# Kernel optimization log

Hardware: AMD Instinct MI355X
Metric: run time of the kernel (lower is better)

## Reference

```python
import jax, jax.numpy as jnp
import numpy as np

GAMMA = 0.99
N_CODES = 1024  # module hardcodes self.N = 2**10

def setup_inputs() -> dict:
    key = jax.random.key(0)
    k1, k2, k3, k4 = jax.random.split(key, 4)
    B, D, S = 16, 256, 2048
    N_q = 8
    return {
        "data_object": jax.random.normal(k1, (B, D, S), dtype=jnp.float32),
        "codebooks": jax.random.normal(k2, (N_q, N_CODES, D), dtype=jnp.float32),
        "N_i": jax.random.uniform(k3, (N_q, N_CODES), dtype=jnp.float32),
        "m_i": jax.random.normal(k4, (N_q, N_CODES, D), dtype=jnp.float32),
    }

def reference(data_object, codebooks, N_i, m_i):
    # data_object: [b, D, s] -> y: [b, s, D]
    b, D, s = data_object.shape
    y = jnp.transpose(data_object, (0, 2, 1))

    def stage(carry, xs):
        residual, cur_y = carry          # [b, s, D] each
        W, Ni, mi = xs                   # [N, D], [N], [N, D]
        flat = residual.reshape(-1, D)   # [b*s, D]
        d2 = (jnp.sum(flat * flat, axis=-1, keepdims=True)
              + jnp.sum(W * W, axis=-1)[None, :]
              - 2.0 * flat @ W.T)
        idx = jnp.argmin(d2, axis=-1)    # [b*s]
        Q = W[idx].reshape(residual.shape)
        # EMA codebook statistics (bincount + index_add as segment sums)
        counts = jax.ops.segment_sum(jnp.ones(idx.shape, flat.dtype), idx, num_segments=N_CODES)
        vec = jax.ops.segment_sum(flat, idx, num_segments=N_CODES)
        new_N = Ni * GAMMA + counts * (1.0 - GAMMA)
        new_m = mi * GAMMA + vec * (1.0 - GAMMA)
        new_W = new_m / jnp.clip(new_N, 1e-8)[:, None]
        return (residual - Q, cur_y + Q), (idx.reshape(b, s), new_N, new_m, new_W)

    init = (y, jnp.zeros_like(y))
    (residual, cur_y), (indices, new_N, new_m, new_W) = jax.lax.scan(
        stage, init, (codebooks, N_i, m_i))

    # straight-through estimator + commitment loss
    logits = y + jax.lax.stop_gradient(cur_y - y)       # [b, s, D]
    commitment_loss = jnp.mean((jax.lax.stop_gradient(cur_y) - y) ** 2)
    logits = jnp.transpose(logits, (0, 2, 1))           # back to [b, D, s]
    return logits, commitment_loss, indices, new_N, new_m, new_W
```

## Files before the change

kernel.cpp:

```cpp
#include <hip/hip_runtime.h>
#include <hip/hip_bf16.h>


using f16   = _Float16;
using f16x4 = __attribute__((ext_vector_type(4))) _Float16;
using f16x8 = __attribute__((ext_vector_type(8))) _Float16;
using f32x4 = __attribute__((ext_vector_type(4))) float;
typedef unsigned long long u64;

#define GAMMA_F 0.99f
#define OMG_F   0.01f
#define LO_SCALE 1024.0f
#define LO_INV   (1.0f/1024.0f)

__global__ void sentinel_kernel(float* out, float v){
  if (threadIdx.x == 0 && blockIdx.x == 0) out[0] = v;
}

__global__ __launch_bounds__(64) void rownorm_kernel(const float* __restrict__ X,
                                                     float* __restrict__ out, int rows){
  int r = blockIdx.x;
  if (r >= rows) return;
  int l = threadIdx.x;
  const float* x = X + (size_t)r * 256;
  float s = 0.f;
  #pragma unroll
  for (int i = 0; i < 4; i++){ float v = x[l + i*64]; s += v*v; }
  #pragma unroll
  for (int o = 32; o > 0; o >>= 1) s += __shfl_down(s, o, 64);
  if (l == 0) out[r] = s;
}

__global__ __launch_bounds__(64) void wsplit_kernel(const float* __restrict__ W,
                                                    f16* __restrict__ frag){
  int blk = blockIdx.x;
  int lane = threadIdx.x;
  int code = (blk >> 3 << 4) + (lane & 15);
  int k0   = (blk & 7)*32 + (lane >> 4)*8;
  const float* src = W + (size_t)code * 256 + k0;
  float4 a = *(const float4*)(src);
  float4 b = *(const float4*)(src + 4);
  float x[8] = {a.x,a.y,a.z,a.w, b.x,b.y,b.z,b.w};
  f16x8 h8, l8;
  #pragma unroll
  for (int i = 0; i < 8; i++){
    f16 h = (f16)x[i];
    h8[i] = h;
    l8[i] = (f16)((x[i] - (float)h) * LO_SCALE);
  }
  f16* dst = frag + (size_t)blk * 1024 + lane*8;
  *(f16x8*)dst         = h8;
  *(f16x8*)(dst + 512) = l8;
}

__global__ __launch_bounds__(256) void init_kernel(const float* __restrict__ data,
                                                   f16* __restrict__ AH, f16* __restrict__ AL,
                                                   float* __restrict__ rnorm){
  __shared__ float rs[32][257];
  __shared__ float nrmp[32][8];
  int blk = blockIdx.x, b = blk >> 6, s0 = (blk & 63) * 32;
  int tid = threadIdx.x, c = tid & 31, g = tid >> 5;
  const float* dptr = data + (size_t)b * 524288 + s0;
  float np_ = 0.f;
  #pragma unroll 8
  for (int dd = 0; dd < 32; ++dd){
    int d = g*32 + dd;
    float x = dptr[(size_t)d * 2048 + c];
    rs[c][d] = x;
    np_ += x*x;
  }
  nrmp[c][g] = np_;
  __syncthreads();
  if (tid < 32){
    float s = 0.f;
    #pragma unroll
    for (int gg = 0; gg < 8; ++gg) s += nrmp[tid][gg];
    rnorm[blk*32 + tid] = s;
  }
  int r0 = blk*32;
  int c2 = tid >> 3, k0 = (tid & 7) * 32;
  #pragma unroll
  for (int jc = 0; jc < 4; ++jc){
    f16x8 h8, l8;
    #pragma unroll
    for (int j = 0; j < 8; ++j){
      float x = rs[c2][k0 + jc*8 + j];
      f16 h = (f16)x;
      h8[j] = h;
      l8[j] = (f16)((x - (float)h) * LO_SCALE);
    }
    size_t off = (size_t)(r0 + c2) * 256 + k0 + jc*8;
    *(f16x8*)(AH + off) = h8;
    *(f16x8*)(AL + off) = l8;
  }
}

__global__ __launch_bounds__(256) void out4init_kernel(const float* __restrict__ mi,
                                                       float* __restrict__ out4){
  int e4 = blockIdx.x*256 + threadIdx.x;
  float4 v = ((const float4*)mi)[e4];
  v.x *= GAMMA_F; v.y *= GAMMA_F; v.z *= GAMMA_F; v.w *= GAMMA_F;
  ((float4*)out4)[e4] = v;
}

__global__ __launch_bounds__(256, 2) void dist_kernel(
    const f16* __restrict__ AH, const f16* __restrict__ AL,
    const f16* __restrict__ whl, const float* __restrict__ wnorm,
    const float* __restrict__ rnorm, u64* __restrict__ keybuf, int q)
{
  __shared__ f16 Bs[2][16384];
  const int tid = threadIdx.x;
  const int lane = tid & 63;
  const int w = tid >> 6;
  const int rb = blockIdx.x, cs = blockIdx.y;
  const int rlo = lane & 15, kg = lane >> 4;
  const int T0 = rb*8 + w*2;

  f16x8 aH[2][8], aL[2][8];
  #pragma unroll
  for (int rt = 0; rt < 2; ++rt)
    #pragma unroll
    for (int kf = 0; kf < 8; ++kf){
      size_t off = (size_t)((T0+rt)*16 + rlo) * 256 + kf*32 + kg*8;
      aH[rt][kf] = *(const f16x8*)(AH + off);
      aL[rt][kf] = *(const f16x8*)(AL + off);
    }
  float rn[2][4];
  #pragma unroll
  for (int rt = 0; rt < 2; ++rt)
    #pragma unroll
    for (int i = 0; i < 4; ++i)
      rn[rt][i] = rnorm[(T0+rt)*16 + kg*4 + i];

  const f16* wb = whl + (size_t)q * 524288;
  const float* wn = wnorm + (q << 10);
  const int ct0 = cs * 16;

  float bestv[8]; int besti[8];
  #pragma unroll
  for (int r8_ = 0; r8_ < 8; ++r8_){ bestv[r8_] = 3.4e38f; besti[r8_] = 0; }

  {
    const f16* src = wb + (size_t)ct0 * 8192;
    f16x8 st[8];
    #pragma unroll
    for (int j = 0; j < 8; ++j) st[j] = *(const f16x8*)(src + tid*8 + j*2048);
    #pragma unroll
    for (int j = 0; j < 8; ++j) *(f16x8*)(&Bs[0][0] + tid*8 + j*2048) = st[j];
  }

  for (int it = 0; it < 8; ++it){
    int cb = ct0 + it*2;
    __syncthreads();
    f16x8 nx[8];
    if (it < 7){
      const f16* src = wb + (size_t)(cb+2) * 8192;
      #pragma unroll
      for (int j = 0; j < 8; ++j) nx[j] = *(const f16x8*)(src + tid*8 + j*2048);
    }
    #pragma unroll
    for (int sub = 0; sub < 2; ++sub){
      const f16* bb = &Bs[it & 1][0] + sub*8192;
      f32x4 hh[2], cr[2];
      #pragma unroll
      for (int rt = 0; rt < 2; ++rt){ hh[rt] = (f32x4)0.0f; cr[rt] = (f32x4)0.0f; }
      __builtin_amdgcn_s_setprio(1);
      #pragma unroll
      for (int kf = 0; kf < 8; ++kf){
        f16x8 bh = *(const f16x8*)(bb + kf*1024 + lane*8);
        f16x8 bl = *(const f16x8*)(bb + kf*1024 + 512 + lane*8);
        hh[0] = __builtin_amdgcn_mfma_f32_16x16x32_f16(aH[0][kf], bh, hh[0], 0,0,0);
        cr[0] = __builtin_amdgcn_mfma_f32_16x16x32_f16(aH[0][kf], bl, cr[0], 0,0,0);
        cr[0] = __builtin_amdgcn_mfma_f32_16x16x32_f16(aL[0][kf], bh, cr[0], 0,0,0);
        hh[1] = __builtin_amdgcn_mfma_f32_16x16x32_f16(aH[1][kf], bh, hh[1], 0,0,0);
        cr[1] = __builtin_amdgcn_mfma_f32_16x16x32_f16(aH[1][kf], bl, cr[1], 0,0,0);
        cr[1] = __builtin_amdgcn_mfma_f32_16x16x32_f16(aL[1][kf], bh, cr[1], 0,0,0);
      }
      __builtin_amdgcn_s_setprio(0);
      int code = ((cb + sub) << 4) + rlo;
      float wnc = wn[code];
      #pragma unroll
      for (int rt = 0; rt < 2; ++rt)
        #pragma unroll
        for (int i = 0; i < 4; ++i){
          float dot = hh[rt][i] + cr[rt][i] * LO_INV;
          float d2 = (rn[rt][i] + wnc) - 2.0f * dot;
          int r8_ = rt*4 + i;
          if (d2 < bestv[r8_] || (d2 == bestv[r8_] && code < besti[r8_])){
            bestv[r8_] = d2; besti[r8_] = code;
          }
        }
    }
    if (it < 7){
      #pragma unroll
      for (int j = 0; j < 8; ++j) *(f16x8*)(&Bs[(it+1) & 1][0] + tid*8 + j*2048) = nx[j];
    }
  }

  #pragma unroll
  for (int off = 1; off <= 8; off <<= 1){
    #pragma unroll
    for (int r8_ = 0; r8_ < 8; ++r8_){
      float ov = __shfl_xor(bestv[r8_], off, 16);
      int   oi = __shfl_xor(besti[r8_], off, 16);
      if (ov < bestv[r8_] || (ov == bestv[r8_] && oi < besti[r8_])){
        bestv[r8_] = ov; besti[r8_] = oi;
      }
    }
  }
  if (rlo == 0){
    #pragma unroll
    for (int r8_ = 0; r8_ < 8; ++r8_){
      int rt = r8_ >> 2, i = r8_ & 3;
      int grow = (T0 + rt)*16 + kg*4 + i;
      unsigned fb = __float_as_uint(bestv[r8_]);
      fb = (fb & 0x80000000u) ? ~fb : (fb | 0x80000000u);
      u64 key = ((u64)fb << 32) | (unsigned)besti[r8_];
      atomicMin(keybuf + grow, key);
    }
  }
}

__global__ __launch_bounds__(256) void hist_kernel(u64* __restrict__ keybuf,
                                                   float* __restrict__ out2q,
                                                   unsigned short* __restrict__ blockhist){
  __shared__ int h[1024];
  int tid = threadIdx.x, b = blockIdx.x;
  #pragma unroll
  for (int i = 0; i < 4; ++i) h[tid + 256*i] = 0;
  __syncthreads();
  #pragma unroll
  for (int j = 0; j < 4; ++j){
    int row = b*1024 + tid + 256*j;
    u64 k = keybuf[row];
    keybuf[row] = ~0ull;
    int c = (int)(k & 0xFFFF);
    out2q[row] = (float)c;
    atomicAdd(&h[c], 1);
  }
  __syncthreads();
  #pragma unroll
  for (int i = 0; i < 4; ++i)
    blockhist[b*1024 + tid + 256*i] = (unsigned short)h[tid + 256*i];
}

__global__ __launch_bounds__(256) void scanscatter_kernel(
    const unsigned short* __restrict__ blockhist, const float* __restrict__ out2q,
    unsigned short* __restrict__ rowlist, const float* __restrict__ Ni,
    float* __restrict__ out3, int q)
{
  __shared__ int wtot[4];
  __shared__ int cur[1024];
  int tid = threadIdx.x, b = blockIdx.x, lane = tid & 63, w = tid >> 6;
  const ushort4* bh4 = (const ushort4*)blockhist;
  int tot[4] = {0,0,0,0}, pre[4] = {0,0,0,0};
  for (int bb = 0; bb < 32; ++bb){
    ushort4 h = bh4[bb*256 + tid];
    if (bb < b){ pre[0]+=h.x; pre[1]+=h.y; pre[2]+=h.z; pre[3]+=h.w; }
    tot[0]+=h.x; tot[1]+=h.y; tot[2]+=h.z; tot[3]+=h.w;
  }
  int s = tot[0]+tot[1]+tot[2]+tot[3];
  int v = s;
  #pragma unroll
  for (int d = 1; d < 64; d <<= 1){
    int o = __shfl_up(v, d, 64);
    if (lane >= d) v += o;
  }
  if (lane == 63) wtot[w] = v;
  __syncthreads();
  int woff = 0;
  #pragma unroll
  for (int ww = 0; ww < 4; ++ww) if (ww < w) woff += wtot[ww];
  int base = woff + v - s;
  if (b == 0){
    const int qb = q << 10;
    out3[qb + 4*tid+0] = Ni[qb + 4*tid+0]*GAMMA_F + (float)tot[0]*OMG_F;
    out3[qb + 4*tid+1] = Ni[qb + 4*tid+1]*GAMMA_F + (float)tot[1]*OMG_F;
    out3[qb + 4*tid+2] = Ni[qb + 4*tid+2]*GAMMA_F + (float)tot[2]*OMG_F;
    out3[qb + 4*tid+3] = Ni[qb + 4*tid+3]*GAMMA_F + (float)tot[3]*OMG_F;
  }
  cur[4*tid+0] = base + pre[0];
  cur[4*tid+1] = base + tot[0] + pre[1];
  cur[4*tid+2] = base + tot[0]+tot[1] + pre[2];
  cur[4*tid+3] = base + tot[0]+tot[1]+tot[2] + pre[3];
  __syncthreads();
  #pragma unroll
  for (int j = 0; j < 4; ++j){
    int row = b*1024 + tid + 256*j;
    int c = (int)out2q[row];
    int pos = atomicAdd(&cur[c], 1);
    rowlist[pos] = (unsigned short)row;
  }
}

__global__ __launch_bounds__(64) void update_kernel(
    f16* __restrict__ AH, f16* __restrict__ AL,
    const unsigned short* __restrict__ rowlist, const float* __restrict__ out2q,
    const float* __restrict__ codebooks, float* __restrict__ out4,
    float* __restrict__ rnorm, int q)
{
  const int lane = threadIdx.x;
  const int s0 = blockIdx.x * 16;
  int myrow = 0, mycode = 0;
  if (lane < 16){
    myrow = rowlist[s0 + lane];
    mycode = (int)out2q[myrow];
  }
  float vs[4] = {0.f, 0.f, 0.f, 0.f};
  float Wk[4] = {0.f, 0.f, 0.f, 0.f};
  int prev = -1;
  int rowp = __shfl(myrow, 0, 64);
  f16x4 ph = *(const f16x4*)(AH + (size_t)rowp*256 + lane*4);
  f16x4 pl = *(const f16x4*)(AL + (size_t)rowp*256 + lane*4);
  for (int s = 0; s < 16; ++s){
    int row  = __shfl(myrow, s, 64);
    int code = __shfl(mycode, s, 64);
    f16x4 h4 = ph, l4 = pl;
    if (s < 15){
      int rown = __shfl(myrow, s+1, 64);
      ph = *(const f16x4*)(AH + (size_t)rown*256 + lane*4);
      pl = *(const f16x4*)(AL + (size_t)rown*256 + lane*4);
    }
    if (code != prev){
      if (prev >= 0){
        float* dst = out4 + (((size_t)q << 10) + prev)*256 + lane*4;
        #pragma unroll
        for (int t = 0; t < 4; ++t) atomicAdd(dst + t, vs[t] * OMG_F);
      }
      float4 wv = *(const float4*)&codebooks[(((size_t)q << 10) + code)*256 + lane*4];
      Wk[0] = wv.x; Wk[1] = wv.y; Wk[2] = wv.z; Wk[3] = wv.w;
      vs[0] = vs[1] = vs[2] = vs[3] = 0.f;
      prev = code;
    }
    size_t base = (size_t)row * 256 + lane*4;
    f16x4 nh, nl;
    float p = 0.f;
    #pragma unroll
    for (int t = 0; t < 4; ++t){
      float rj = (float)h4[t] + (float)l4[t] * LO_INV;
      vs[t] += rj;
      float rn_ = rj - Wk[t];
      f16 hh = (f16)rn_;
      nh[t] = hh;
      nl[t] = (f16)((rn_ - (float)hh) * LO_SCALE);
      p += rn_ * rn_;
    }
    *(f16x4*)(AH + base) = nh;
    *(f16x4*)(AL + base) = nl;
    #pragma unroll
    for (int o = 32; o > 0; o >>= 1) p += __shfl_down(p, o, 64);
    if (lane == 0) rnorm[row] = p;
  }
  if (prev >= 0){
    float* dst = out4 + (((size_t)q << 10) + prev)*256 + lane*4;
    #pragma unroll
    for (int t = 0; t < 4; ++t) atomicAdd(dst + t, vs[t] * OMG_F);
  }
}

__global__ __launch_bounds__(256) void logits_loss_kernel(
    const float* __restrict__ data, const f16* __restrict__ AH, const f16* __restrict__ AL,
    float* __restrict__ out0, float* __restrict__ out1)
{
  __shared__ float rs[32][257];
  int blk = blockIdx.x, b = blk >> 6, s0 = (blk & 63) * 32;
  int tid = threadIdx.x;
  int r0 = blk*32;
  int c2 = tid >> 3, k0 = (tid & 7) * 32;
  #pragma unroll
  for (int jc = 0; jc < 4; ++jc){
    size_t off = (size_t)(r0 + c2) * 256 + k0 + jc*8;
    f16x8 h8 = *(const f16x8*)(AH + off);
    f16x8 l8 = *(const f16x8*)(AL + off);
    #pragma unroll
    for (int j = 0; j < 8; ++j)
      rs[c2][k0 + jc*8 + j] = (float)h8[j] + (float)l8[j] * LO_INV;
  }
  __syncthreads();
  int c = tid & 31, g = tid >> 5;
  const float* dptr = data + (size_t)b * 524288 + s0;
  float* optr = out0 + (size_t)b * 524288 + s0;
  float lsum = 0.f;
  #pragma unroll 8
  for (int dd = 0; dd < 32; ++dd){
    int d = g*32 + dd;
    float r = rs[c][d];
    lsum += r*r;
    optr[(size_t)d * 2048 + c] = dptr[(size_t)d * 2048 + c] - r;
  }
  #pragma unroll
  for (int o = 32; o > 0; o >>= 1) lsum += __shfl_down(lsum, o, 64);
  if ((tid & 63) == 0) atomicAdd(out1, lsum * (1.0f / 8388608.0f));
}

__global__ __launch_bounds__(256) void out5_kernel(const float* __restrict__ out4,
                                                   const float* __restrict__ out3,
                                                   float* __restrict__ out5){
  int e4 = blockIdx.x*256 + threadIdx.x;
  float Nn = fmaxf(out3[e4 >> 6], 1e-8f);
  float4 v = ((const float4*)out4)[e4];
  v.x /= Nn; v.y /= Nn; v.z /= Nn; v.w /= Nn;
  ((float4*)out5)[e4] = v;
}

extern "C" void kernel_launch(void* const* d_in, const int* in_sizes, int n_in,
                              void* d_out, int out_size, void* d_ws, size_t ws_size,
                              hipStream_t stream){
  float* out = (float*)d_out;

  const float* data = nullptr; const float* codebooks = nullptr;
  const float* Ni = nullptr;   const float* mi = nullptr;
  for (int i = 0; i < n_in; ++i){
    if      (in_sizes[i] == 8388608) data = (const float*)d_in[i];
    else if (in_sizes[i] == 8192)    Ni   = (const float*)d_in[i];
    else if (in_sizes[i] == 2097152){
      if (!codebooks) codebooks = (const float*)d_in[i];
      else            mi        = (const float*)d_in[i];
    }
  }
  if (!data || !codebooks || !Ni || !mi){
    sentinel_kernel<<<1, 64, 0, stream>>>(out, 6666.0f);
    return;
  }

  const size_t ws_need = 42500096ull;
  if (ws_size < ws_need){
    sentinel_kernel<<<1, 64, 0, stream>>>(out, 7777.0f);
    return;
  }
  f16*   AH     = (f16*)d_ws;
  f16*   AL     = AH + 8388608;
  f16*   whl    = AL + 8388608;
  float* wnormb = (float*)(whl + 4194304);
  float* rnorm  = wnormb + 8192;
  unsigned short* blockhist = (unsigned short*)(rnorm + 32768);
  unsigned short* rowlist   = blockhist + 32768;
  u64*   keybuf = (u64*)(rowlist + 32768);

  float* out0 = out;
  float* out1 = out0 + 8388608;
  float* out2 = out1 + 1;
  float* out3 = out2 + 262144;
  float* out4 = out3 + 8192;
  float* out5 = out4 + 2097152;

  hipMemsetAsync(out1, 0, sizeof(float), stream);
  hipMemsetAsync(keybuf, 0xFF, 262144, stream);

  wsplit_kernel<<<dim3(4096), 64, 0, stream>>>(codebooks, whl);
  rownorm_kernel<<<dim3(8192), 64, 0, stream>>>(codebooks, wnormb, 8192);
  init_kernel<<<dim3(1024), 256, 0, stream>>>(data, AH, AL, rnorm);
  out4init_kernel<<<dim3(2048), 256, 0, stream>>>(mi, out4);

  for (int q = 0; q < 8; ++q){
    float* out2q = out2 + (size_t)q * 32768;
    dist_kernel<<<dim3(256, 4), 256, 0, stream>>>(AH, AL, whl, wnormb, rnorm, keybuf, q);
    hist_kernel<<<dim3(32), 256, 0, stream>>>(keybuf, out2q, blockhist);
    scanscatter_kernel<<<dim3(32), 256, 0, stream>>>(blockhist, out2q, rowlist,
                                                     Ni, out3, q);
    update_kernel<<<dim3(2048), 64, 0, stream>>>(AH, AL, rowlist, out2q,
                                                 codebooks, out4, rnorm, q);
  }

  logits_loss_kernel<<<dim3(1024), 256, 0, stream>>>(data, AH, AL, out0, out1);
  out5_kernel<<<dim3(2048), 256, 0, stream>>>(out4, out3, out5);
}
```

Before: 904.7 us.

## Use direct global-to-LDS loads in dist kernel and fold last-stage residual into logits

The distance kernel now stages codebook tiles with global_load_lds, writing straight into shared memory instead of going through registers and separate LDS stores. The update kernel is templated so the final stage skips rewriting the residual and its norm. The last-stage subtraction of the selected codeword moves into the logits/loss kernel instead. The update kernel also processes 8 rows per block instead of 16, doubling the grid size. This cuts register pressure and redundant memory traffic, but relies on the LDS layout matching the per-wave offset (w*512) used by global_load_lds.

```diff
diff --git a/kernel.cpp b/kernel.cpp
--- a/kernel.cpp
+++ b/kernel.cpp
@@ -7,11 +7,18 @@
 using f16x8 = __attribute__((ext_vector_type(8))) _Float16;
 using f32x4 = __attribute__((ext_vector_type(4))) float;
 typedef unsigned long long u64;
+typedef unsigned int u32;
 
 #define GAMMA_F 0.99f
 #define OMG_F   0.01f
 #define LO_SCALE 1024.0f
 #define LO_INV   (1.0f/1024.0f)
+
+__device__ __forceinline__ void gload16(const void* g, void* l){
+  __builtin_amdgcn_global_load_lds(
+      (const __attribute__((address_space(1))) u32*)g,
+      (__attribute__((address_space(3))) u32*)l, 16, 0, 0);
+}
 
 __global__ void sentinel_kernel(float* out, float v){
   if (threadIdx.x == 0 && blockIdx.x == 0) out[0] = v;
@@ -141,22 +148,22 @@
   for (int r8_ = 0; r8_ < 8; ++r8_){ bestv[r8_] = 3.4e38f; besti[r8_] = 0; }
 
   {
-    const f16* src = wb + (size_t)ct0 * 8192;
-    f16x8 st[8];
-    #pragma unroll
-    for (int j = 0; j < 8; ++j) st[j] = *(const f16x8*)(src + tid*8 + j*2048);
-    #pragma unroll
-    for (int j = 0; j < 8; ++j) *(f16x8*)(&Bs[0][0] + tid*8 + j*2048) = st[j];
+    const f16* src = wb + (size_t)ct0 * 8192 + tid*8;
+    f16* dst = &Bs[0][0] + w*512;
+    #pragma unroll
+    for (int j = 0; j < 8; ++j)
+      gload16(src + j*2048, dst + j*2048);
   }
 
   for (int it = 0; it < 8; ++it){
     int cb = ct0 + it*2;
     __syncthreads();
-    f16x8 nx[8];
     if (it < 7){
-      const f16* src = wb + (size_t)(cb+2) * 8192;
+      const f16* src = wb + (size_t)(cb+2) * 8192 + tid*8;
+      f16* dst = &Bs[(it+1) & 1][0] + w*512;
       #pragma unroll
-      for (int j = 0; j < 8; ++j) nx[j] = *(const f16x8*)(src + tid*8 + j*2048);
+      for (int j = 0; j < 8; ++j)
+        gload16(src + j*2048, dst + j*2048);
     }
     #pragma unroll
     for (int sub = 0; sub < 2; ++sub){
@@ -191,10 +198,6 @@
           }
         }
     }
-    if (it < 7){
-      #pragma unroll
-      for (int j = 0; j < 8; ++j) *(f16x8*)(&Bs[(it+1) & 1][0] + tid*8 + j*2048) = nx[j];
-    }
   }
 
   #pragma unroll
@@ -293,6 +296,7 @@
   }
 }
 
+template<int LAST>
 __global__ __launch_bounds__(64) void update_kernel(
     f16* __restrict__ AH, f16* __restrict__ AL,
     const unsigned short* __restrict__ rowlist, const float* __restrict__ out2q,
@@ -300,9 +304,9 @@
     float* __restrict__ rnorm, int q)
 {
   const int lane = threadIdx.x;
-  const int s0 = blockIdx.x * 16;
+  const int s0 = blockIdx.x * 8;
   int myrow = 0, mycode = 0;
-  if (lane < 16){
+  if (lane < 8){
     myrow = rowlist[s0 + lane];
     mycode = (int)out2q[myrow];
   }
@@ -312,11 +316,11 @@
   int rowp = __shfl(myrow, 0, 64);
   f16x4 ph = *(const f16x4*)(AH + (size_t)rowp*256 + lane*4);
   f16x4 pl = *(const f16x4*)(AL + (size_t)rowp*256 + lane*4);
-  for (int s = 0; s < 16; ++s){
+  for (int s = 0; s < 8; ++s){
     int row  = __shfl(myrow, s, 64);
     int code = __shfl(mycode, s, 64);
     f16x4 h4 = ph, l4 = pl;
-    if (s < 15){
+    if (s < 7){
       int rown = __shfl(myrow, s+1, 64);
       ph = *(const f16x4*)(AH + (size_t)rown*256 + lane*4);
       pl = *(const f16x4*)(AL + (size_t)rown*256 + lane*4);
@@ -327,29 +331,35 @@
         #pragma unroll
         for (int t = 0; t < 4; ++t) atomicAdd(dst + t, vs[t] * OMG_F);
       }
-      float4 wv = *(const float4*)&codebooks[(((size_t)q << 10) + code)*256 + lane*4];
-      Wk[0] = wv.x; Wk[1] = wv.y; Wk[2] = wv.z; Wk[3] = wv.w;
+      if (!LAST){
+        float4 wv = *(const float4*)&codebooks[(((size_t)q << 10) + code)*256 + lane*4];
+        Wk[0] = wv.x; Wk[1] = wv.y; Wk[2] = wv.z; Wk[3] = wv.w;
+      }
       vs[0] = vs[1] = vs[2] = vs[3] = 0.f;
       prev = code;
     }
-    size_t base = (size_t)row * 256 + lane*4;
+    float p = 0.f;
     f16x4 nh, nl;
-    float p = 0.f;
     #pragma unroll
     for (int t = 0; t < 4; ++t){
       float rj = (float)h4[t] + (float)l4[t] * LO_INV;
       vs[t] += rj;
-      float rn_ = rj - Wk[t];
-      f16 hh = (f16)rn_;
-      nh[t] = hh;
-      nl[t] = (f16)((rn_ - (float)hh) * LO_SCALE);
-      p += rn_ * rn_;
-    }
-    *(f16x4*)(AH + base) = nh;
-    *(f16x4*)(AL + base) = nl;
-    #pragma unroll
-    for (int o = 32; o > 0; o >>= 1) p += __shfl_down(p, o, 64);
-    if (lane == 0) rnorm[row] = p;
+      if (!LAST){
+        float rn_ = rj - Wk[t];
+        f16 hh = (f16)rn_;
+        nh[t] = hh;
+        nl[t] = (f16)((rn_ - (float)hh) * LO_SCALE);
+        p += rn_ * rn_;
+      }
+    }
+    if (!LAST){
+      size_t base = (size_t)row * 256 + lane*4;
+      *(f16x4*)(AH + base) = nh;
+      *(f16x4*)(AL + base) = nl;
+      #pragma unroll
+      for (int o = 32; o > 0; o >>= 1) p += __shfl_down(p, o, 64);
+      if (lane == 0) rnorm[row] = p;
+    }
   }
   if (prev >= 0){
     float* dst = out4 + (((size_t)q << 10) + prev)*256 + lane*4;
@@ -360,6 +370,7 @@
 
 __global__ __launch_bounds__(256) void logits_loss_kernel(
     const float* __restrict__ data, const f16* __restrict__ AH, const f16* __restrict__ AL,
+    const float* __restrict__ out2q7, const float* __restrict__ W7,
     float* __restrict__ out0, float* __restrict__ out1)
 {
   __shared__ float rs[32][257];
@@ -367,14 +378,20 @@
   int tid = threadIdx.x;
   int r0 = blk*32;
   int c2 = tid >> 3, k0 = (tid & 7) * 32;
+  int grow = r0 + c2;
+  int code = (int)out2q7[grow];
+  const float* wrow = W7 + (size_t)code * 256 + k0;
   #pragma unroll
   for (int jc = 0; jc < 4; ++jc){
-    size_t off = (size_t)(r0 + c2) * 256 + k0 + jc*8;
+    size_t off = (size_t)grow * 256 + k0 + jc*8;
     f16x8 h8 = *(const f16x8*)(AH + off);
     f16x8 l8 = *(const f16x8*)(AL + off);
+    float4 w0 = *(const float4*)(wrow + jc*8);
+    float4 w1 = *(const float4*)(wrow + jc*8 + 4);
+    float wv[8] = {w0.x,w0.y,w0.z,w0.w, w1.x,w1.y,w1.z,w1.w};
     #pragma unroll
     for (int j = 0; j < 8; ++j)
-      rs[c2][k0 + jc*8 + j] = (float)h8[j] + (float)l8[j] * LO_INV;
+      rs[c2][k0 + jc*8 + j] = ((float)h8[j] + (float)l8[j] * LO_INV) - wv[j];
   }
   __syncthreads();
   int c = tid & 31, g = tid >> 5;
@@ -458,10 +475,17 @@
     hist_kernel<<<dim3(32), 256, 0, stream>>>(keybuf, out2q, blockhist);
     scanscatter_kernel<<<dim3(32), 256, 0, stream>>>(blockhist, out2q, rowlist,
                                                      Ni, out3, q);
-    update_kernel<<<dim3(2048), 64, 0, stream>>>(AH, AL, rowlist, out2q,
-                                                 codebooks, out4, rnorm, q);
-  }
-
-  logits_loss_kernel<<<dim3(1024), 256, 0, stream>>>(data, AH, AL, out0, out1);
+    if (q < 7)
+      update_kernel<0><<<dim3(4096), 64, 0, stream>>>(AH, AL, rowlist, out2q,
+                                                      codebooks, out4, rnorm, q);
+    else
+      update_kernel<1><<<dim3(4096), 64, 0, stream>>>(AH, AL, rowlist, out2q,
+                                                      codebooks, out4, rnorm, q);
+  }
+
+  logits_loss_kernel<<<dim3(1024), 256, 0, stream>>>(data, AH, AL,
+                                                     out2 + 7*32768,
+                                                     codebooks + 7*262144,
+                                                     out0, out1);
   out5_kernel<<<dim3(2048), 256, 0, stream>>>(out4, out3, out5);
 }
```

After: 958.8 us. 6.0% more time.
